# Kernel tuning notes

Hardware: AMD Instinct MI355X
Metric: run time of the kernel (lower is better)

Reference implementation:

```python
import jax, jax.numpy as jnp
import numpy as np

VOCAB = 50257
WORD_DIM = 300
HIDDEN = 256
BATCH = 256   # number of trees
LEAVES = 1024  # leaves per complete binary tree (power of 2)


def setup_inputs() -> dict:
    key = jax.random.key(0)
    k_ids, k_emb, k_w1, k_b1, k_w2, k_b2 = jax.random.split(key, 6)
    word_ids = jax.random.randint(k_ids, (BATCH, LEAVES), 0, VOCAB)
    emb_table = jax.random.normal(k_emb, (VOCAB, WORD_DIM), dtype=jnp.float32) * 0.1
    W1 = jax.random.normal(k_w1, (WORD_DIM, HIDDEN), dtype=jnp.float32) * (1.0 / np.sqrt(WORD_DIM))
    b1 = jax.random.normal(k_b1, (HIDDEN,), dtype=jnp.float32) * 0.01
    W2 = jax.random.normal(k_w2, (2 * HIDDEN, HIDDEN), dtype=jnp.float32) * (1.0 / np.sqrt(2 * HIDDEN))
    b2 = jax.random.normal(k_b2, (HIDDEN,), dtype=jnp.float32) * 0.01
    return {"word_ids": word_ids, "emb_table": emb_table, "W1": W1, "b1": b1, "W2": W2, "b2": b2}


def reference(word_ids, emb_table, W1, b1, W2, b2):
    # Leaves: embedding lookup + word2hidden linear (no nonlinearity, as in source)
    h = jnp.einsum('blw,wh->blh', emb_table[word_ids], W1) + b1  # [B, L, H]
    # Internal nodes: concat(left, right) @ W2 + b2, level by level up the
    # complete binary tree. Loop count = log2(LEAVES), a small static constant.
    while h.shape[1] > 1:
        B, n, H = h.shape
        pairs = h.reshape(B, n // 2, 2 * H)  # concat of sibling states
        h = jnp.einsum('bnk,kh->bnh', pairs, W2) + b2
    return h[:, 0, :]  # root hidden state per tree: [B, H]
```

## Files before the change

kernel.cpp:

```cpp
#include <hip/hip_runtime.h>
#include <hip/hip_bf16.h>
#include <stdint.h>

#define VOCAB 50257
#define WD 300
#define KP1 320
#define MP 50432

using bf16 = __hip_bfloat16;
typedef __attribute__((ext_vector_type(4))) float f32x4;
typedef __attribute__((ext_vector_type(8))) short bf16x8;

__device__ __forceinline__ void async_load16(const void* g, void* l) {
    __builtin_amdgcn_global_load_lds(
        (const __attribute__((address_space(1))) uint32_t*)(uintptr_t)g,
        (__attribute__((address_space(3))) uint32_t*)l, 16, 0, 0);
}

__global__ void prep_w(const float* __restrict__ W1, const float* __restrict__ W2,
                       const float* __restrict__ b2,
                       bf16* __restrict__ w1t, bf16* __restrict__ w2t,
                       bf16* __restrict__ w2b, float* __restrict__ b4,
                       float* __restrict__ zbuf) {
    if (blockIdx.x == 1344) {
        __shared__ float b2s[256];
        int n = threadIdx.x;
        b2s[n] = b2[n];
        zbuf[n] = 0.0f;
        __syncthreads();
        float acc = b2s[n];
        #pragma unroll 8
        for (int k = 0; k < 256; ++k)
            acc += b2s[k] * (W2[k * 256 + n] + W2[(k + 256) * 256 + n]);
        b4[n] = acc;
        return;
    }
    int idx = blockIdx.x * 256 + threadIdx.x;
    if (idx < 256 * KP1) {
        int n = idx / KP1;
        int k = idx - n * KP1;
        w1t[idx] = __float2bfloat16(k < WD ? W1[k * 256 + n] : 0.0f);
    } else if (idx < 256 * KP1 + 131072) {
        int j = idx - 256 * KP1;
        int n = j >> 9, k = j & 511;
        w2t[j] = __float2bfloat16(W2[k * 256 + n]);
    } else {
        int j = idx - 256 * KP1 - 131072;
        w2b[j] = __float2bfloat16(W2[j]);
    }
}

template <int AMODE, bool OUT_F32>
__device__ __forceinline__ void tile_gemm(
    char* smem, const void* Av, const int* ids,
    const bf16* BT, int Bstr, const float* bias,
    void* C, int Cs, int coff, int K, int As, int m0,
    const float* zbuf)
{
    constexpr int ASZ = (AMODE == 2) ? 16384 : 8192;
    constexpr int BSZ = 16384, STAGE = ASZ + BSZ;

    const int t = threadIdx.x, w = t >> 6, lane = t & 63;
    const int rg = w >> 2, cgr = w & 3, mi = lane & 15, q = lane >> 4;
    const bf16* Ab = (const bf16*)Av;

    int4 idq = {0, 0, 0, 0};
    if constexpr (AMODE == 1) idq = ((const int4*)ids)[m0 + (t >> 2)];

    auto stage = [&](int ke, int buf) {
        char* Asm = smem + buf * STAGE;
        char* Bsm = Asm + ASZ;
        if constexpr (AMODE == 2) {
            const float* A32 = (const float*)Av;
            #pragma unroll
            for (int i = 0; i < 2; ++i) {
                int s = i * 512 + t;
                int row = s >> 3;
                int kcd = (s & 7) ^ (row & 7);
                int k = ke + kcd * 4;
                int grow = m0 + row; if (grow >= VOCAB) grow = VOCAB - 1;
                const float* g = (k <= 296) ? (A32 + (size_t)grow * WD + k) : zbuf;
                async_load16(g, Asm + i * 8192 + w * 1024);
            }
        } else {
            int row = t >> 2;
            int kcd = (t & 3) ^ ((row >> 2) & 3);
            const bf16* g;
            if constexpr (AMODE == 1) {
                int sel = ke >> 8;
                int id = (sel & 2) ? ((sel & 1) ? idq.w : idq.z)
                                   : ((sel & 1) ? idq.y : idq.x);
                g = Ab + (size_t)id * 256 + (ke & 255) + kcd * 8;
            } else {
                g = Ab + (size_t)(m0 + row) * As + ke + kcd * 8;
            }
            async_load16(g, Asm + w * 1024);
        }
        #pragma unroll
        for (int i = 0; i < 2; ++i) {
            int s = i * 512 + t;
            int col = s >> 2;
            int kcd = (s & 3) ^ ((col >> 2) & 3);
            async_load16(BT + (size_t)col * Bstr + ke + kcd * 8,
                         Bsm + i * 8192 + w * 1024);
        }
    };

    f32x4 acc[4][4] = {};

    auto compute = [&](int buf) {
        const char* Asm = smem + buf * STAGE;
        const bf16* Bs16 = (const bf16*)(Asm + ASZ);
        bf16x8 af[4], bfr[4];
        if constexpr (AMODE == 2) {
            const float* As32 = (const float*)Asm;
            #pragma unroll
            for (int r = 0; r < 4; ++r) {
                int row = rg * 64 + r * 16 + mi;
                int sl = row * 8 + ((2 * q) ^ (row & 7));
                f32x4 lo = *(const f32x4*)(As32 + sl * 4);
                f32x4 hi = *(const f32x4*)(As32 + (sl ^ 1) * 4);
                union { bf16x8 v; bf16 hh[8]; } u;
                #pragma unroll
                for (int j = 0; j < 4; ++j) u.hh[j] = __float2bfloat16(lo[j]);
                #pragma unroll
                for (int j = 0; j < 4; ++j) u.hh[4 + j] = __float2bfloat16(hi[j]);
                af[r] = u.v;
            }
        } else {
            const bf16* As16 = (const bf16*)Asm;
            #pragma unroll
            for (int r = 0; r < 4; ++r) {
                int row = rg * 64 + r * 16 + mi;
                int slot = row * 4 + (q ^ ((row >> 2) & 3));
                af[r] = *(const bf16x8*)(As16 + slot * 8);
            }
        }
        #pragma unroll
        for (int c = 0; c < 4; ++c) {
            int col = cgr * 64 + c * 16 + mi;
            int slot = col * 4 + (q ^ ((col >> 2) & 3));
            bfr[c] = *(const bf16x8*)(Bs16 + slot * 8);
        }
        #pragma unroll
        for (int r = 0; r < 4; ++r)
            #pragma unroll
            for (int c = 0; c < 4; ++c)
                acc[r][c] = __builtin_amdgcn_mfma_f32_16x16x32_bf16(af[r], bfr[c], acc[r][c], 0, 0, 0);
    };

    const int S = K >> 5;
    if constexpr (AMODE == 2) {
        stage(0, 0);
        for (int k0 = 0; k0 < S; ++k0) {
            if (k0 + 1 < S) {
                stage((k0 + 1) * 32, (k0 + 1) & 1);
                asm volatile("s_waitcnt vmcnt(4)\n\ts_barrier" ::: "memory");
            } else {
                asm volatile("s_waitcnt vmcnt(0)\n\ts_barrier" ::: "memory");
            }
            compute(k0 & 1);
            asm volatile("s_waitcnt lgkmcnt(0)\n\ts_barrier" ::: "memory");
        }
    } else {
        stage(0, 0);
        if (S > 1) stage(32, 1);
        for (int k0 = 0; k0 < S; ++k0) {
            if (k0 + 1 < S)
                asm volatile("s_waitcnt vmcnt(3)\n\ts_barrier" ::: "memory");
            else
                asm volatile("s_waitcnt vmcnt(0)\n\ts_barrier" ::: "memory");
            if (k0 + 2 < S) stage((k0 + 2) * 32, (k0 + 2) % 3);
            compute(k0 % 3);
        }
    }

    #pragma unroll
    for (int r = 0; r < 4; ++r) {
        int rowb = m0 + rg * 64 + r * 16 + q * 4;
        #pragma unroll
        for (int c = 0; c < 4; ++c) {
            int col = cgr * 64 + c * 16 + mi;
            float bv = bias[col];
            #pragma unroll
            for (int i = 0; i < 4; ++i) {
                float v = acc[r][c][i] + bv;
                size_t o = (size_t)(rowb + i) * Cs + coff + col;
                if (OUT_F32) ((float*)C)[o] = v;
                else         ((bf16*)C)[o] = __float2bfloat16(v);
            }
        }
    }
}

__global__ __launch_bounds__(512)
void combo(const float* __restrict__ emb, const bf16* __restrict__ w1t,
           const float* __restrict__ b1, const bf16* __restrict__ w2t,
           const bf16* __restrict__ w2b, bf16* __restrict__ w4t,
           bf16* __restrict__ proj, const float* __restrict__ zbuf) {
    __shared__ char smem[73728];
    int blk = blockIdx.x;
    if (blk < 8) {
        int j = blk >> 1, s = blk & 1;
        tile_gemm<0, false>(smem, w2t + 256 * (j >> 1), nullptr,
                            w2b + 65536 * (j & 1), 256, zbuf,
                            w4t, 1024, 256 * j, 256, 512, s * 128, nullptr);
    } else {
        tile_gemm<2, false>(smem, emb, nullptr, w1t, KP1, b1,
                            proj, 256, 0, KP1, WD, (blk - 8) * 128, zbuf);
    }
}

__global__ __launch_bounds__(512)
void mainK(const bf16* __restrict__ proj, const int* __restrict__ ids,
           const bf16* __restrict__ w4t, const float* __restrict__ b4,
           bf16* __restrict__ h) {
    __shared__ char smem[73728];
    tile_gemm<1, false>(smem, proj, ids, w4t, 1024, b4,
                        h, 256, 0, 1024, 256, blockIdx.x * 128, nullptr);
}

__global__ __launch_bounds__(512)
void treeK(const bf16* __restrict__ h, const bf16* __restrict__ w4t,
           const float* __restrict__ b4, float* __restrict__ out) {
    constexpr int ASZ = 8192, BSZ = 16384, STAGE = ASZ + BSZ;
    __shared__ char smem[3 * STAGE];
    __shared__ bf16 Ht[128 * 256];
    __shared__ bf16 Ht2[32 * 256];
    __shared__ bf16 Ht3[8 * 256];

    const int t = threadIdx.x, w = t >> 6, lane = t & 63;
    const int rg = w >> 2, cgr = w & 3, mi = lane & 15, q = lane >> 4;
    const int b = blockIdx.x;
    const int m0 = b * 128;

    {
        auto stageA = [&](int ke, int buf) {
            char* Asm = smem + buf * STAGE;
            char* Bsm = Asm + ASZ;
            int row = t >> 2;
            int kcd = (t & 3) ^ ((row >> 2) & 3);
            async_load16(h + (size_t)(m0 + row) * 1024 + ke + kcd * 8, Asm + w * 1024);
            #pragma unroll
            for (int i = 0; i < 2; ++i) {
                int s = i * 512 + t;
                int col = s >> 2;
                int kcd2 = (s & 3) ^ ((col >> 2) & 3);
                async_load16(w4t + (size_t)col * 1024 + ke + kcd2 * 8,
                             Bsm + i * 8192 + w * 1024);
            }
        };
        f32x4 acc[4][4] = {};
        stageA(0, 0); stageA(32, 1);
        for (int k0i = 0; k0i < 32; ++k0i) {
            if (k0i + 1 < 32)
                asm volatile("s_waitcnt vmcnt(3)\n\ts_barrier" ::: "memory");
            else
                asm volatile("s_waitcnt vmcnt(0)\n\ts_barrier" ::: "memory");
            if (k0i + 2 < 32) stageA((k0i + 2) * 32, (k0i + 2) % 3);
            const bf16* As16 = (const bf16*)(smem + (k0i % 3) * STAGE);
            const bf16* Bs16 = (const bf16*)(smem + (k0i % 3) * STAGE + ASZ);
            bf16x8 af[4], bfr[4];
            #pragma unroll
            for (int r = 0; r < 4; ++r) {
                int row = rg * 64 + r * 16 + mi;
                int slot = row * 4 + (q ^ ((row >> 2) & 3));
                af[r] = *(const bf16x8*)(As16 + slot * 8);
            }
            #pragma unroll
            for (int c = 0; c < 4; ++c) {
                int col = cgr * 64 + c * 16 + mi;
                int slot = col * 4 + (q ^ ((col >> 2) & 3));
                bfr[c] = *(const bf16x8*)(Bs16 + slot * 8);
            }
            #pragma unroll
            for (int r = 0; r < 4; ++r)
                #pragma unroll
                for (int c = 0; c < 4; ++c)
                    acc[r][c] = __builtin_amdgcn_mfma_f32_16x16x32_bf16(af[r], bfr[c], acc[r][c], 0, 0, 0);
        }
        #pragma unroll
        for (int r = 0; r < 4; ++r) {
            int rowb = rg * 64 + r * 16 + q * 4;
            #pragma unroll
            for (int c = 0; c < 4; ++c) {
                int col = cgr * 64 + c * 16 + mi;
                float bv = b4[col];
                int chunk = col >> 3;
                #pragma unroll
                for (int i = 0; i < 4; ++i) {
                    int row = rowb + i;
                    Ht[(row * 32 + (chunk ^ (row & 31))) * 8 + (col & 7)] =
                        __float2bfloat16(acc[r][c][i] + bv);
                }
            }
        }
    }
    __syncthreads();

    auto stageF = [&](int ke, int buf) {
        char* Bb = smem + buf * 32768;
        #pragma unroll
        for (int sub = 0; sub < 2; ++sub)
            #pragma unroll
            for (int i = 0; i < 2; ++i) {
                int s = i * 512 + t;
                int col = s >> 2;
                int kcd = (s & 3) ^ ((col >> 2) & 3);
                async_load16(w4t + (size_t)col * 1024 + ke + sub * 32 + kcd * 8,
                             Bb + sub * 16384 + i * 8192 + w * 1024);
            }
    };

    {
        f32x4 acc2[4] = {};
        stageF(0, 0);
        for (int r = 0; r < 16; ++r) {
            if (r + 1 < 16) {
                stageF((r + 1) * 64, (r + 1) & 1);
                asm volatile("s_waitcnt vmcnt(4)\n\ts_barrier" ::: "memory");
            } else {
                asm volatile("s_waitcnt vmcnt(0)\n\ts_barrier" ::: "memory");
            }
            const bf16* Bb = (const bf16*)(smem + (r & 1) * 32768);
            #pragma unroll
            for (int sub = 0; sub < 2; ++sub) {
                int k0 = r * 64 + sub * 32;
                int n = rg * 16 + mi;
                int r2 = 4 * n + (k0 >> 8);
                int kc = ((k0 & 255) >> 3) + q;
                bf16x8 a = *(const bf16x8*)(Ht + (r2 * 32 + (kc ^ (r2 & 31))) * 8);
                #pragma unroll
                for (int c = 0; c < 4; ++c) {
                    int col = cgr * 64 + c * 16 + mi;
                    int slot = col * 4 + (q ^ ((col >> 2) & 3));
                    bf16x8 bb = *(const bf16x8*)(Bb + sub * 8192 + slot * 8);
                    acc2[c] = __builtin_amdgcn_mfma_f32_16x16x32_bf16(a, bb, acc2[c], 0, 0, 0);
                }
            }
            asm volatile("s_waitcnt lgkmcnt(0)\n\ts_barrier" ::: "memory");
        }
        #pragma unroll
        for (int c = 0; c < 4; ++c) {
            int col = cgr * 64 + c * 16 + mi;
            float bv = b4[col];
            int chunk = col >> 3;
            #pragma unroll
            for (int i = 0; i < 4; ++i) {
                int row = rg * 16 + q * 4 + i;
                Ht2[(row * 32 + (chunk ^ (row & 31))) * 8 + (col & 7)] =
                    __float2bfloat16(acc2[c][i] + bv);
            }
        }
    }
    __syncthreads();

    {
        f32x4 acc3[4] = {};
        stageF(0, 0);
        for (int r = 0; r < 16; ++r) {
            if (r + 1 < 16) {
                stageF((r + 1) * 64, (r + 1) & 1);
                asm volatile("s_waitcnt vmcnt(4)\n\ts_barrier" ::: "memory");
            } else {
                asm volatile("s_waitcnt vmcnt(0)\n\ts_barrier" ::: "memory");
            }
            const bf16* Bb = (const bf16*)(smem + (r & 1) * 32768);
            #pragma unroll
            for (int sub = 0; sub < 2; ++sub) {
                int k0 = r * 64 + sub * 32;
                int r3 = (4 * mi + (k0 >> 8)) & 31;
                int kc = ((k0 & 255) >> 3) + q;
                bf16x8 a = *(const bf16x8*)(Ht2 + (r3 * 32 + (kc ^ (r3 & 31))) * 8);
                #pragma unroll
                for (int c = 0; c < 4; ++c) {
                    int col = cgr * 64 + c * 16 + mi;
                    int slot = col * 4 + (q ^ ((col >> 2) & 3));
                    bf16x8 bb = *(const bf16x8*)(Bb + sub * 8192 + slot * 8);
                    acc3[c] = __builtin_amdgcn_mfma_f32_16x16x32_bf16(a, bb, acc3[c], 0, 0, 0);
                }
            }
            asm volatile("s_waitcnt lgkmcnt(0)\n\ts_barrier" ::: "memory");
        }
        if (rg == 0 && q < 2) {
            #pragma unroll
            for (int c = 0; c < 4; ++c) {
                int col = cgr * 64 + c * 16 + mi;
                float bv = b4[col];
                #pragma unroll
                for (int i = 0; i < 4; ++i)
                    Ht3[(q * 4 + i) * 256 + col] = __float2bfloat16(acc3[c][i] + bv);
            }
        }
    }
    __syncthreads();

    {
        f32x4 acc4[4] = {};
        stageF(0, 0);
        for (int r = 0; r < 16; ++r) {
            if (r + 1 < 16) {
                stageF((r + 1) * 64, (r + 1) & 1);
                asm volatile("s_waitcnt vmcnt(4)\n\ts_barrier" ::: "memory");
            } else {
                asm volatile("s_waitcnt vmcnt(0)\n\ts_barrier" ::: "memory");
            }
            const bf16* Bb = (const bf16*)(smem + (r & 1) * 32768);
            #pragma unroll
            for (int sub = 0; sub < 2; ++sub) {
                int k0 = r * 64 + sub * 32;
                int r4 = (4 * (mi & 1) + (k0 >> 8)) & 7;
                bf16x8 a = *(const bf16x8*)(Ht3 + r4 * 256 + (k0 & 255) + q * 8);
                #pragma unroll
                for (int c = 0; c < 4; ++c) {
                    int col = cgr * 64 + c * 16 + mi;
                    int slot = col * 4 + (q ^ ((col >> 2) & 3));
                    bf16x8 bb = *(const bf16x8*)(Bb + sub * 8192 + slot * 8);
                    acc4[c] = __builtin_amdgcn_mfma_f32_16x16x32_bf16(a, bb, acc4[c], 0, 0, 0);
                }
            }
            asm volatile("s_waitcnt lgkmcnt(0)\n\ts_barrier" ::: "memory");
        }
        if (rg == 0 && q == 0) {
            #pragma unroll
            for (int c = 0; c < 4; ++c) {
                int col = cgr * 64 + c * 16 + mi;
                float bv = b4[col];
                #pragma unroll
                for (int i = 0; i < 2; ++i)
                    out[(size_t)(b * 2 + i) * 256 + col] = acc4[c][i] + bv;
            }
        }
    }
}

extern "C" void kernel_launch(void* const* d_in, const int* in_sizes, int n_in,
                              void* d_out, int out_size, void* d_ws, size_t ws_size,
                              hipStream_t stream) {
    const int*   ids = (const int*)d_in[0];
    const float* emb = (const float*)d_in[1];
    const float* W1  = (const float*)d_in[2];
    const float* b1  = (const float*)d_in[3];
    const float* W2  = (const float*)d_in[4];
    const float* b2  = (const float*)d_in[5];
    (void)in_sizes; (void)n_in; (void)out_size; (void)ws_size;

    char* ws = (char*)d_ws;
    size_t off = 0;
    float* zbuf = (float*)(ws + off); off += 1024;
    float* b4   = (float*)(ws + off); off += 1024;
    bf16* w1t = (bf16*)(ws + off); off += (size_t)256 * KP1 * 2;
    bf16* w2t = (bf16*)(ws + off); off += (size_t)256 * 512 * 2;
    bf16* w2b = (bf16*)(ws + off); off += (size_t)512 * 256 * 2;
    bf16* w4t = (bf16*)(ws + off); off += (size_t)256 * 1024 * 2;
    bf16* proj = (bf16*)(ws + off); off += (size_t)MP * 256 * 2;
    bf16* h  = (bf16*)(ws + off); off += (size_t)65536 * 256 * 2;
    (void)off;

    prep_w<<<1345, 256, 0, stream>>>(W1, W2, b2, w1t, w2t, w2b, b4, zbuf);

    combo<<<402, 512, 0, stream>>>(emb, w1t, b1, w2t, w2b, w4t, proj, zbuf);

    mainK<<<512, 512, 0, stream>>>(proj, ids, w4t, b4, h);

    treeK<<<128, 512, 0, stream>>>(h, w4t, b4, (float*)d_out);
}
```

Baseline: 220.9 us.

## Split fused tree kernel into split-K tail GEMMs with atomic accumulation

Replaces the single 128-block tree kernel, which reduced four levels serially inside each block, with four launches of a generic tail GEMM. Each launch splits K across blocks and accumulates fp32 partials into zeroed buffers with atomics, so more blocks run per level. Later levels read fp32 input and convert it to bf16 on the fly. The cost is extra launches, two memsets, atomic traffic and fp32 intermediates in global memory, and the proj buffer is reused as scratch.

```diff
diff --git a/kernel.cpp b/kernel.cpp
--- a/kernel.cpp
+++ b/kernel.cpp
@@ -220,86 +220,45 @@
                         h, 256, 0, 1024, 256, blockIdx.x * 128, nullptr);
 }
 
+template <bool INF32>
 __global__ __launch_bounds__(512)
-void treeK(const bf16* __restrict__ h, const bf16* __restrict__ w4t,
-           const float* __restrict__ b4, float* __restrict__ out) {
-    constexpr int ASZ = 8192, BSZ = 16384, STAGE = ASZ + BSZ;
-    __shared__ char smem[3 * STAGE];
-    __shared__ bf16 Ht[128 * 256];
-    __shared__ bf16 Ht2[32 * 256];
-    __shared__ bf16 Ht3[8 * 256];
+void tailK(const void* __restrict__ inv, const bf16* __restrict__ BT,
+           const float* __restrict__ bias, float* __restrict__ out,
+           int RT, int SL) {
+    constexpr int ABYTES = INF32 ? 32768 : 16384;
+    constexpr int STAGE = ABYTES + 32768;
+    __shared__ char smem[2 * STAGE];
 
     const int t = threadIdx.x, w = t >> 6, lane = t & 63;
     const int rg = w >> 2, cgr = w & 3, mi = lane & 15, q = lane >> 4;
-    const int b = blockIdx.x;
-    const int m0 = b * 128;
-
-    {
-        auto stageA = [&](int ke, int buf) {
-            char* Asm = smem + buf * STAGE;
-            char* Bsm = Asm + ASZ;
-            int row = t >> 2;
-            int kcd = (t & 3) ^ ((row >> 2) & 3);
-            async_load16(h + (size_t)(m0 + row) * 1024 + ke + kcd * 8, Asm + w * 1024);
+    const int rt = blockIdx.x % RT, ks = blockIdx.x / RT;
+    const int m0 = rt * 128;
+    const int k0 = ks * SL;
+    const int R = SL >> 6;
+
+    auto stage = [&](int r, int buf) {
+        char* As = smem + buf * STAGE;
+        char* Bs = As + ABYTES;
+        const int kb = k0 + r * 64;
+        if constexpr (INF32) {
+            const float* A32 = (const float*)inv;
+            #pragma unroll
+            for (int i = 0; i < 4; ++i) {
+                int s = i * 512 + t;
+                int row = s >> 4, g = s & 15;
+                async_load16(A32 + (size_t)(m0 + row) * 1024 + kb + ((g ^ (row & 15)) << 2),
+                             As + i * 8192 + w * 1024);
+            }
+        } else {
+            const bf16* A16 = (const bf16*)inv;
             #pragma unroll
             for (int i = 0; i < 2; ++i) {
                 int s = i * 512 + t;
-                int col = s >> 2;
-                int kcd2 = (s & 3) ^ ((col >> 2) & 3);
-                async_load16(w4t + (size_t)col * 1024 + ke + kcd2 * 8,
-                             Bsm + i * 8192 + w * 1024);
-            }
-        };
-        f32x4 acc[4][4] = {};
-        stageA(0, 0); stageA(32, 1);
-        for (int k0i = 0; k0i < 32; ++k0i) {
-            if (k0i + 1 < 32)
-                asm volatile("s_waitcnt vmcnt(3)\n\ts_barrier" ::: "memory");
-            else
-                asm volatile("s_waitcnt vmcnt(0)\n\ts_barrier" ::: "memory");
-            if (k0i + 2 < 32) stageA((k0i + 2) * 32, (k0i + 2) % 3);
-            const bf16* As16 = (const bf16*)(smem + (k0i % 3) * STAGE);
-            const bf16* Bs16 = (const bf16*)(smem + (k0i % 3) * STAGE + ASZ);
-            bf16x8 af[4], bfr[4];
-            #pragma unroll
-            for (int r = 0; r < 4; ++r) {
-                int row = rg * 64 + r * 16 + mi;
-                int slot = row * 4 + (q ^ ((row >> 2) & 3));
-                af[r] = *(const bf16x8*)(As16 + slot * 8);
-            }
-            #pragma unroll
-            for (int c = 0; c < 4; ++c) {
-                int col = cgr * 64 + c * 16 + mi;
-                int slot = col * 4 + (q ^ ((col >> 2) & 3));
-                bfr[c] = *(const bf16x8*)(Bs16 + slot * 8);
-            }
-            #pragma unroll
-            for (int r = 0; r < 4; ++r)
-                #pragma unroll
-                for (int c = 0; c < 4; ++c)
-                    acc[r][c] = __builtin_amdgcn_mfma_f32_16x16x32_bf16(af[r], bfr[c], acc[r][c], 0, 0, 0);
-        }
-        #pragma unroll
-        for (int r = 0; r < 4; ++r) {
-            int rowb = rg * 64 + r * 16 + q * 4;
-            #pragma unroll
-            for (int c = 0; c < 4; ++c) {
-                int col = cgr * 64 + c * 16 + mi;
-                float bv = b4[col];
-                int chunk = col >> 3;
-                #pragma unroll
-                for (int i = 0; i < 4; ++i) {
-                    int row = rowb + i;
-                    Ht[(row * 32 + (chunk ^ (row & 31))) * 8 + (col & 7)] =
-                        __float2bfloat16(acc[r][c][i] + bv);
-                }
-            }
-        }
-    }
-    __syncthreads();
-
-    auto stageF = [&](int ke, int buf) {
-        char* Bb = smem + buf * 32768;
+                int row = s >> 3, c = s & 7;
+                async_load16(A16 + (size_t)(m0 + row) * 1024 + kb + ((c ^ (row & 7)) << 3),
+                             As + i * 8192 + w * 1024);
+            }
+        }
         #pragma unroll
         for (int sub = 0; sub < 2; ++sub)
             #pragma unroll
@@ -307,129 +266,78 @@
                 int s = i * 512 + t;
                 int col = s >> 2;
                 int kcd = (s & 3) ^ ((col >> 2) & 3);
-                async_load16(w4t + (size_t)col * 1024 + ke + sub * 32 + kcd * 8,
-                             Bb + sub * 16384 + i * 8192 + w * 1024);
+                async_load16(BT + (size_t)col * 1024 + kb + sub * 32 + kcd * 8,
+                             Bs + sub * 16384 + i * 8192 + w * 1024);
             }
     };
 
-    {
-        f32x4 acc2[4] = {};
-        stageF(0, 0);
-        for (int r = 0; r < 16; ++r) {
-            if (r + 1 < 16) {
-                stageF((r + 1) * 64, (r + 1) & 1);
-                asm volatile("s_waitcnt vmcnt(4)\n\ts_barrier" ::: "memory");
-            } else {
-                asm volatile("s_waitcnt vmcnt(0)\n\ts_barrier" ::: "memory");
-            }
-            const bf16* Bb = (const bf16*)(smem + (r & 1) * 32768);
-            #pragma unroll
-            for (int sub = 0; sub < 2; ++sub) {
-                int k0 = r * 64 + sub * 32;
-                int n = rg * 16 + mi;
-                int r2 = 4 * n + (k0 >> 8);
-                int kc = ((k0 & 255) >> 3) + q;
-                bf16x8 a = *(const bf16x8*)(Ht + (r2 * 32 + (kc ^ (r2 & 31))) * 8);
+    f32x4 acc[4][4] = {};
+
+    auto compute = [&](int buf) {
+        const char* As = smem + buf * STAGE;
+        const bf16* Bs16 = (const bf16*)(As + ABYTES);
+        #pragma unroll
+        for (int kk = 0; kk < 2; ++kk) {
+            bf16x8 af[4], bfr[4];
+            #pragma unroll
+            for (int r = 0; r < 4; ++r) {
+                int row = rg * 64 + r * 16 + mi;
+                if constexpr (INF32) {
+                    const float* A32 = (const float*)As;
+                    int g0 = kk * 8 + q * 2;
+                    f32x4 lo = *(const f32x4*)(A32 + (row * 16 + (g0 ^ (row & 15))) * 4);
+                    f32x4 hi = *(const f32x4*)(A32 + (row * 16 + ((g0 + 1) ^ (row & 15))) * 4);
+                    union { bf16x8 v; bf16 hh[8]; } u;
+                    #pragma unroll
+                    for (int j = 0; j < 4; ++j) u.hh[j] = __float2bfloat16(lo[j]);
+                    #pragma unroll
+                    for (int j = 0; j < 4; ++j) u.hh[4 + j] = __float2bfloat16(hi[j]);
+                    af[r] = u.v;
+                } else {
+                    const bf16* A16 = (const bf16*)As;
+                    int c = kk * 4 + q;
+                    af[r] = *(const bf16x8*)(A16 + (row * 8 + (c ^ (row & 7))) * 8);
+                }
+            }
+            #pragma unroll
+            for (int c4 = 0; c4 < 4; ++c4) {
+                int col = cgr * 64 + c4 * 16 + mi;
+                int slot = col * 4 + (q ^ ((col >> 2) & 3));
+                bfr[c4] = *(const bf16x8*)(Bs16 + kk * 8192 + slot * 8);
+            }
+            #pragma unroll
+            for (int r = 0; r < 4; ++r)
                 #pragma unroll
-                for (int c = 0; c < 4; ++c) {
-                    int col = cgr * 64 + c * 16 + mi;
-                    int slot = col * 4 + (q ^ ((col >> 2) & 3));
-                    bf16x8 bb = *(const bf16x8*)(Bb + sub * 8192 + slot * 8);
-                    acc2[c] = __builtin_amdgcn_mfma_f32_16x16x32_bf16(a, bb, acc2[c], 0, 0, 0);
-                }
-            }
-            asm volatile("s_waitcnt lgkmcnt(0)\n\ts_barrier" ::: "memory");
-        }
-        #pragma unroll
-        for (int c = 0; c < 4; ++c) {
-            int col = cgr * 64 + c * 16 + mi;
-            float bv = b4[col];
-            int chunk = col >> 3;
-            #pragma unroll
-            for (int i = 0; i < 4; ++i) {
-                int row = rg * 16 + q * 4 + i;
-                Ht2[(row * 32 + (chunk ^ (row & 31))) * 8 + (col & 7)] =
-                    __float2bfloat16(acc2[c][i] + bv);
-            }
-        }
-    }
-    __syncthreads();
-
-    {
-        f32x4 acc3[4] = {};
-        stageF(0, 0);
-        for (int r = 0; r < 16; ++r) {
-            if (r + 1 < 16) {
-                stageF((r + 1) * 64, (r + 1) & 1);
-                asm volatile("s_waitcnt vmcnt(4)\n\ts_barrier" ::: "memory");
-            } else {
-                asm volatile("s_waitcnt vmcnt(0)\n\ts_barrier" ::: "memory");
-            }
-            const bf16* Bb = (const bf16*)(smem + (r & 1) * 32768);
-            #pragma unroll
-            for (int sub = 0; sub < 2; ++sub) {
-                int k0 = r * 64 + sub * 32;
-                int r3 = (4 * mi + (k0 >> 8)) & 31;
-                int kc = ((k0 & 255) >> 3) + q;
-                bf16x8 a = *(const bf16x8*)(Ht2 + (r3 * 32 + (kc ^ (r3 & 31))) * 8);
-                #pragma unroll
-                for (int c = 0; c < 4; ++c) {
-                    int col = cgr * 64 + c * 16 + mi;
-                    int slot = col * 4 + (q ^ ((col >> 2) & 3));
-                    bf16x8 bb = *(const bf16x8*)(Bb + sub * 8192 + slot * 8);
-                    acc3[c] = __builtin_amdgcn_mfma_f32_16x16x32_bf16(a, bb, acc3[c], 0, 0, 0);
-                }
-            }
-            asm volatile("s_waitcnt lgkmcnt(0)\n\ts_barrier" ::: "memory");
-        }
-        if (rg == 0 && q < 2) {
-            #pragma unroll
-            for (int c = 0; c < 4; ++c) {
-                int col = cgr * 64 + c * 16 + mi;
-                float bv = b4[col];
-                #pragma unroll
-                for (int i = 0; i < 4; ++i)
-                    Ht3[(q * 4 + i) * 256 + col] = __float2bfloat16(acc3[c][i] + bv);
-            }
-        }
-    }
-    __syncthreads();
-
-    {
-        f32x4 acc4[4] = {};
-        stageF(0, 0);
-        for (int r = 0; r < 16; ++r) {
-            if (r + 1 < 16) {
-                stageF((r + 1) * 64, (r + 1) & 1);
-                asm volatile("s_waitcnt vmcnt(4)\n\ts_barrier" ::: "memory");
-            } else {
-                asm volatile("s_waitcnt vmcnt(0)\n\ts_barrier" ::: "memory");
-            }
-            const bf16* Bb = (const bf16*)(smem + (r & 1) * 32768);
-            #pragma unroll
-            for (int sub = 0; sub < 2; ++sub) {
-                int k0 = r * 64 + sub * 32;
-                int r4 = (4 * (mi & 1) + (k0 >> 8)) & 7;
-                bf16x8 a = *(const bf16x8*)(Ht3 + r4 * 256 + (k0 & 255) + q * 8);
-                #pragma unroll
-                for (int c = 0; c < 4; ++c) {
-                    int col = cgr * 64 + c * 16 + mi;
-                    int slot = col * 4 + (q ^ ((col >> 2) & 3));
-                    bf16x8 bb = *(const bf16x8*)(Bb + sub * 8192 + slot * 8);
-                    acc4[c] = __builtin_amdgcn_mfma_f32_16x16x32_bf16(a, bb, acc4[c], 0, 0, 0);
-                }
-            }
-            asm volatile("s_waitcnt lgkmcnt(0)\n\ts_barrier" ::: "memory");
-        }
-        if (rg == 0 && q == 0) {
-            #pragma unroll
-            for (int c = 0; c < 4; ++c) {
-                int col = cgr * 64 + c * 16 + mi;
-                float bv = b4[col];
-                #pragma unroll
-                for (int i = 0; i < 2; ++i)
-                    out[(size_t)(b * 2 + i) * 256 + col] = acc4[c][i] + bv;
-            }
+                for (int c4 = 0; c4 < 4; ++c4)
+                    acc[r][c4] = __builtin_amdgcn_mfma_f32_16x16x32_bf16(af[r], bfr[c4], acc[r][c4], 0, 0, 0);
+        }
+    };
+
+    stage(0, 0);
+    for (int r = 0; r < R; ++r) {
+        if (r + 1 < R) {
+            stage(r + 1, (r + 1) & 1);
+            if constexpr (INF32)
+                asm volatile("s_waitcnt vmcnt(8)\n\ts_barrier" ::: "memory");
+            else
+                asm volatile("s_waitcnt vmcnt(6)\n\ts_barrier" ::: "memory");
+        } else {
+            asm volatile("s_waitcnt vmcnt(0)\n\ts_barrier" ::: "memory");
+        }
+        compute(r & 1);
+        asm volatile("s_waitcnt lgkmcnt(0)\n\ts_barrier" ::: "memory");
+    }
+
+    #pragma unroll
+    for (int r = 0; r < 4; ++r) {
+        int rowb = m0 + rg * 64 + r * 16 + q * 4;
+        #pragma unroll
+        for (int c4 = 0; c4 < 4; ++c4) {
+            int col = cgr * 64 + c4 * 16 + mi;
+            float bv = (ks == 0) ? bias[col] : 0.0f;
+            #pragma unroll
+            for (int i = 0; i < 4; ++i)
+                unsafeAtomicAdd(out + (size_t)(rowb + i) * 256 + col, acc[r][c4][i] + bv);
         }
     }
 }
@@ -457,11 +365,21 @@
     bf16* h  = (bf16*)(ws + off); off += (size_t)65536 * 256 * 2;
     (void)off;
 
+    float* t1f = (float*)proj;
+    float* t2f = t1f + (size_t)16384 * 256;
+    float* t3f = t2f + (size_t)4096 * 256;
+
     prep_w<<<1345, 256, 0, stream>>>(W1, W2, b2, w1t, w2t, w2b, b4, zbuf);
 
     combo<<<402, 512, 0, stream>>>(emb, w1t, b1, w2t, w2b, w4t, proj, zbuf);
 
     mainK<<<512, 512, 0, stream>>>(proj, ids, w4t, b4, h);
 
-    treeK<<<128, 512, 0, stream>>>(h, w4t, b4, (float*)d_out);
-}
+    hipMemsetAsync(t1f, 0, (size_t)(16384 + 4096 + 1024) * 256 * sizeof(float), stream);
+    hipMemsetAsync(d_out, 0, (size_t)256 * 256 * sizeof(float), stream);
+
+    tailK<false><<<256, 512, 0, stream>>>(h,   w4t, b4, t1f, 128, 512);
+    tailK<true ><<<128, 512, 0, stream>>>(t1f, w4t, b4, t2f,  32, 256);
+    tailK<true ><<< 64, 512, 0, stream>>>(t2f, w4t, b4, t3f,   8, 128);
+    tailK<true ><<< 16, 512, 0, stream>>>(t3f, w4t, b4, (float*)d_out, 2, 128);
+}
```

Measured after the change: 258.9 us. +17.2%, slower.

## Load W4 fragments directly from global and remap waves to column slices

Applied to the files above, without the earlier changes.

The last three tree-level GEMMs stop staging the combined weight matrix into LDS with double-buffered async loads and barriers. Each wave now owns a 32-column slice and reads its B fragments straight from global memory (likely L2-resident), while A fragments still come from the shared hidden-state buffers. This removes the per-step barriers and the LDS traffic for B, and avoids redundant MFMA work in the small upper levels. In exchange each wave issues uncoalesced global loads inside the MFMA loop, with no software pipelining to hide their latency.

```diff
diff --git a/kernel.cpp b/kernel.cpp
--- a/kernel.cpp
+++ b/kernel.cpp
@@ -298,137 +298,88 @@
     }
     __syncthreads();
 
-    auto stageF = [&](int ke, int buf) {
-        char* Bb = smem + buf * 32768;
-        #pragma unroll
-        for (int sub = 0; sub < 2; ++sub)
-            #pragma unroll
-            for (int i = 0; i < 2; ++i) {
-                int s = i * 512 + t;
-                int col = s >> 2;
-                int kcd = (s & 3) ^ ((col >> 2) & 3);
-                async_load16(w4t + (size_t)col * 1024 + ke + sub * 32 + kcd * 8,
-                             Bb + sub * 16384 + i * 8192 + w * 1024);
-            }
-    };
+    const int c0w = w * 32;
+    const bf16* Bg0 = w4t + (size_t)(c0w + mi) * 1024 + q * 8;
+    const bf16* Bg1 = w4t + (size_t)(c0w + 16 + mi) * 1024 + q * 8;
 
     {
-        f32x4 acc2[4] = {};
-        stageF(0, 0);
-        for (int r = 0; r < 16; ++r) {
-            if (r + 1 < 16) {
-                stageF((r + 1) * 64, (r + 1) & 1);
-                asm volatile("s_waitcnt vmcnt(4)\n\ts_barrier" ::: "memory");
-            } else {
-                asm volatile("s_waitcnt vmcnt(0)\n\ts_barrier" ::: "memory");
-            }
-            const bf16* Bb = (const bf16*)(smem + (r & 1) * 32768);
-            #pragma unroll
-            for (int sub = 0; sub < 2; ++sub) {
-                int k0 = r * 64 + sub * 32;
-                int n = rg * 16 + mi;
-                int r2 = 4 * n + (k0 >> 8);
-                int kc = ((k0 & 255) >> 3) + q;
-                bf16x8 a = *(const bf16x8*)(Ht + (r2 * 32 + (kc ^ (r2 & 31))) * 8);
-                #pragma unroll
-                for (int c = 0; c < 4; ++c) {
-                    int col = cgr * 64 + c * 16 + mi;
-                    int slot = col * 4 + (q ^ ((col >> 2) & 3));
-                    bf16x8 bb = *(const bf16x8*)(Bb + sub * 8192 + slot * 8);
-                    acc2[c] = __builtin_amdgcn_mfma_f32_16x16x32_bf16(a, bb, acc2[c], 0, 0, 0);
+        f32x4 acc[2][2] = {};
+        #pragma unroll 4
+        for (int ks = 0; ks < 32; ++ks) {
+            bf16x8 b0 = *(const bf16x8*)(Bg0 + ks * 32);
+            bf16x8 b1 = *(const bf16x8*)(Bg1 + ks * 32);
+            int kc = (ks & 7) * 4 + q;
+            int r2a = 4 * mi + (ks >> 3);
+            int r2b = 4 * (16 + mi) + (ks >> 3);
+            bf16x8 a0 = *(const bf16x8*)(Ht + (r2a * 32 + (kc ^ (r2a & 31))) * 8);
+            bf16x8 a1 = *(const bf16x8*)(Ht + (r2b * 32 + (kc ^ (r2b & 31))) * 8);
+            acc[0][0] = __builtin_amdgcn_mfma_f32_16x16x32_bf16(a0, b0, acc[0][0], 0, 0, 0);
+            acc[0][1] = __builtin_amdgcn_mfma_f32_16x16x32_bf16(a0, b1, acc[0][1], 0, 0, 0);
+            acc[1][0] = __builtin_amdgcn_mfma_f32_16x16x32_bf16(a1, b0, acc[1][0], 0, 0, 0);
+            acc[1][1] = __builtin_amdgcn_mfma_f32_16x16x32_bf16(a1, b1, acc[1][1], 0, 0, 0);
+        }
+        #pragma unroll
+        for (int f = 0; f < 2; ++f) {
+            #pragma unroll
+            for (int g = 0; g < 2; ++g) {
+                int col = c0w + g * 16 + mi;
+                float bv = b4[col];
+                int chunk = col >> 3;
+                #pragma unroll
+                for (int i = 0; i < 4; ++i) {
+                    int row = f * 16 + q * 4 + i;
+                    Ht2[(row * 32 + (chunk ^ (row & 31))) * 8 + (col & 7)] =
+                        __float2bfloat16(acc[f][g][i] + bv);
                 }
             }
-            asm volatile("s_waitcnt lgkmcnt(0)\n\ts_barrier" ::: "memory");
-        }
-        #pragma unroll
-        for (int c = 0; c < 4; ++c) {
-            int col = cgr * 64 + c * 16 + mi;
-            float bv = b4[col];
-            int chunk = col >> 3;
-            #pragma unroll
-            for (int i = 0; i < 4; ++i) {
-                int row = rg * 16 + q * 4 + i;
-                Ht2[(row * 32 + (chunk ^ (row & 31))) * 8 + (col & 7)] =
-                    __float2bfloat16(acc2[c][i] + bv);
-            }
         }
     }
     __syncthreads();
 
     {
-        f32x4 acc3[4] = {};
-        stageF(0, 0);
-        for (int r = 0; r < 16; ++r) {
-            if (r + 1 < 16) {
-                stageF((r + 1) * 64, (r + 1) & 1);
-                asm volatile("s_waitcnt vmcnt(4)\n\ts_barrier" ::: "memory");
-            } else {
-                asm volatile("s_waitcnt vmcnt(0)\n\ts_barrier" ::: "memory");
-            }
-            const bf16* Bb = (const bf16*)(smem + (r & 1) * 32768);
-            #pragma unroll
-            for (int sub = 0; sub < 2; ++sub) {
-                int k0 = r * 64 + sub * 32;
-                int r3 = (4 * mi + (k0 >> 8)) & 31;
-                int kc = ((k0 & 255) >> 3) + q;
-                bf16x8 a = *(const bf16x8*)(Ht2 + (r3 * 32 + (kc ^ (r3 & 31))) * 8);
-                #pragma unroll
-                for (int c = 0; c < 4; ++c) {
-                    int col = cgr * 64 + c * 16 + mi;
-                    int slot = col * 4 + (q ^ ((col >> 2) & 3));
-                    bf16x8 bb = *(const bf16x8*)(Bb + sub * 8192 + slot * 8);
-                    acc3[c] = __builtin_amdgcn_mfma_f32_16x16x32_bf16(a, bb, acc3[c], 0, 0, 0);
-                }
-            }
-            asm volatile("s_waitcnt lgkmcnt(0)\n\ts_barrier" ::: "memory");
-        }
-        if (rg == 0 && q < 2) {
-            #pragma unroll
-            for (int c = 0; c < 4; ++c) {
-                int col = cgr * 64 + c * 16 + mi;
+        f32x4 acc[2] = {};
+        #pragma unroll 4
+        for (int ks = 0; ks < 32; ++ks) {
+            bf16x8 b0 = *(const bf16x8*)(Bg0 + ks * 32);
+            bf16x8 b1 = *(const bf16x8*)(Bg1 + ks * 32);
+            int kc = (ks & 7) * 4 + q;
+            int r3 = (4 * mi + (ks >> 3)) & 31;
+            bf16x8 a = *(const bf16x8*)(Ht2 + (r3 * 32 + (kc ^ (r3 & 31))) * 8);
+            acc[0] = __builtin_amdgcn_mfma_f32_16x16x32_bf16(a, b0, acc[0], 0, 0, 0);
+            acc[1] = __builtin_amdgcn_mfma_f32_16x16x32_bf16(a, b1, acc[1], 0, 0, 0);
+        }
+        if (q < 2) {
+            #pragma unroll
+            for (int g = 0; g < 2; ++g) {
+                int col = c0w + g * 16 + mi;
                 float bv = b4[col];
                 #pragma unroll
                 for (int i = 0; i < 4; ++i)
-                    Ht3[(q * 4 + i) * 256 + col] = __float2bfloat16(acc3[c][i] + bv);
+                    Ht3[(q * 4 + i) * 256 + col] = __float2bfloat16(acc[g][i] + bv);
             }
         }
     }
     __syncthreads();
 
     {
-        f32x4 acc4[4] = {};
-        stageF(0, 0);
-        for (int r = 0; r < 16; ++r) {
-            if (r + 1 < 16) {
-                stageF((r + 1) * 64, (r + 1) & 1);
-                asm volatile("s_waitcnt vmcnt(4)\n\ts_barrier" ::: "memory");
-            } else {
-                asm volatile("s_waitcnt vmcnt(0)\n\ts_barrier" ::: "memory");
-            }
-            const bf16* Bb = (const bf16*)(smem + (r & 1) * 32768);
-            #pragma unroll
-            for (int sub = 0; sub < 2; ++sub) {
-                int k0 = r * 64 + sub * 32;
-                int r4 = (4 * (mi & 1) + (k0 >> 8)) & 7;
-                bf16x8 a = *(const bf16x8*)(Ht3 + r4 * 256 + (k0 & 255) + q * 8);
-                #pragma unroll
-                for (int c = 0; c < 4; ++c) {
-                    int col = cgr * 64 + c * 16 + mi;
-                    int slot = col * 4 + (q ^ ((col >> 2) & 3));
-                    bf16x8 bb = *(const bf16x8*)(Bb + sub * 8192 + slot * 8);
-                    acc4[c] = __builtin_amdgcn_mfma_f32_16x16x32_bf16(a, bb, acc4[c], 0, 0, 0);
-                }
-            }
-            asm volatile("s_waitcnt lgkmcnt(0)\n\ts_barrier" ::: "memory");
-        }
-        if (rg == 0 && q == 0) {
-            #pragma unroll
-            for (int c = 0; c < 4; ++c) {
-                int col = cgr * 64 + c * 16 + mi;
+        f32x4 acc[2] = {};
+        #pragma unroll 4
+        for (int ks = 0; ks < 32; ++ks) {
+            bf16x8 b0 = *(const bf16x8*)(Bg0 + ks * 32);
+            bf16x8 b1 = *(const bf16x8*)(Bg1 + ks * 32);
+            int r4 = (4 * (mi & 1) + (ks >> 3)) & 7;
+            bf16x8 a = *(const bf16x8*)(Ht3 + r4 * 256 + (ks & 7) * 32 + q * 8);
+            acc[0] = __builtin_amdgcn_mfma_f32_16x16x32_bf16(a, b0, acc[0], 0, 0, 0);
+            acc[1] = __builtin_amdgcn_mfma_f32_16x16x32_bf16(a, b1, acc[1], 0, 0, 0);
+        }
+        if (q == 0) {
+            #pragma unroll
+            for (int g = 0; g < 2; ++g) {
+                int col = c0w + g * 16 + mi;
                 float bv = b4[col];
                 #pragma unroll
                 for (int i = 0; i < 2; ++i)
-                    out[(size_t)(b * 2 + i) * 256 + col] = acc4[c][i] + bv;
+                    out[(size_t)(b * 2 + i) * 256 + col] = acc[g][i] + bv;
             }
         }
     }
```

New measurement: 237.4 us. 1.07x slower.
